# Kernel tuning notes

Measured on AMD Instinct MI355X. Metric: run time of the kernel, lower is better.

## Reference

```python
import jax, jax.numpy as jnp
import numpy as np

D_MODEL = 768
N_HEADS = 4
N_POINTS = 4
PATCH = 16
IMG = 224
HF = IMG // PATCH  # 14
WF = IMG // PATCH  # 14
LQ = HF * WF       # 196 tokens
DH = D_MODEL // N_HEADS  # 192


def setup_inputs() -> dict:
    key = jax.random.key(0)
    ks = jax.random.split(key, 14)
    s = 0.02
    inp = {
        "x": jax.random.normal(ks[0], (4, 16, 3, IMG, IMG), dtype=jnp.float32),
        # patch-embed conv (Conv2d 3->768, k=16, s=16)
        "embed_w": s * jax.random.normal(ks[1], (D_MODEL, 3, PATCH, PATCH), dtype=jnp.float32),
        "embed_b": jnp.zeros((D_MODEL,), dtype=jnp.float32),
        # MSDeformAttn linears (nn.Linear stores W as [out, in]; y = x @ W.T + b)
        "value_w": s * jax.random.normal(ks[2], (D_MODEL, D_MODEL), dtype=jnp.float32),
        "value_b": jnp.zeros((D_MODEL,), dtype=jnp.float32),
        "off_w": s * jax.random.normal(ks[3], (N_HEADS * N_POINTS * 2, D_MODEL), dtype=jnp.float32),
        "off_b": s * jax.random.normal(ks[4], (N_HEADS * N_POINTS * 2,), dtype=jnp.float32),
        "aw_w": s * jax.random.normal(ks[5], (N_HEADS * N_POINTS, D_MODEL), dtype=jnp.float32),
        "aw_b": jnp.zeros((N_HEADS * N_POINTS,), dtype=jnp.float32),
        "outp_w": s * jax.random.normal(ks[6], (D_MODEL, D_MODEL), dtype=jnp.float32),
        "outp_b": jnp.zeros((D_MODEL,), dtype=jnp.float32),
        # final nn.Linear proj
        "proj_w": s * jax.random.normal(ks[7], (D_MODEL, D_MODEL), dtype=jnp.float32),
        "proj_b": jnp.zeros((D_MODEL,), dtype=jnp.float32),
    }
    return inp


def _patch_embed(x, w, b):
    # x: (N,3,H,W); non-overlapping 16x16 patches == Conv2d(3,D,16,16)
    N = x.shape[0]
    xh = x.reshape(N, 3, HF, PATCH, WF, PATCH)
    feat = jnp.einsum('nchpwq,dcpq->nhwd', xh, w) + b  # (N,HF,WF,D)
    return feat.reshape(N, LQ, D_MODEL)


def _ref_points():
    lin = jnp.linspace(0.0, 1.0, HF)
    gy, gx = jnp.meshgrid(lin, lin, indexing='ij')
    return jnp.stack([gx, gy], -1).reshape(LQ, 2)  # (Lq, 2) in [0,1], (x,y)


def _deform_attn_core(value, loc, attn):
    # value: (N, Lq, M, Dh); loc: (N, Lq, M, P, 2) normalized [0,1]; attn: (N, Lq, M, P)
    N = value.shape[0]
    # grid_sample align_corners=False: pixel = (2*loc-1 + 1)*S/2 - 0.5 = loc*S - 0.5
    px = loc[..., 0] * WF - 0.5
    py = loc[..., 1] * HF - 0.5
    x0 = jnp.floor(px).astype(jnp.int32)
    y0 = jnp.floor(py).astype(jnp.int32)
    x1, y1 = x0 + 1, y0 + 1
    wx1 = px - x0.astype(px.dtype)
    wy1 = py - y0.astype(py.dtype)
    wx0, wy0 = 1.0 - wx1, 1.0 - wy1

    valh = value.transpose(0, 2, 1, 3)  # (N, M, HW, Dh)

    def gather(ix, iy):
        valid = (ix >= 0) & (ix < WF) & (iy >= 0) & (iy < HF)  # zeros padding
        idx = jnp.clip(iy, 0, HF - 1) * WF + jnp.clip(ix, 0, WF - 1)
        idxm = idx.transpose(0, 2, 1, 3).reshape(N, N_HEADS, LQ * N_POINTS)
        g = jnp.take_along_axis(valh, idxm[..., None], axis=2)  # (N,M,Lq*P,Dh)
        g = g * valid.transpose(0, 2, 1, 3).reshape(N, N_HEADS, LQ * N_POINTS, 1)
        return g.reshape(N, N_HEADS, LQ, N_POINTS, DH)

    def w4(a, b):  # (N,Lq,M,P) -> (N,M,Lq,P,1)
        return (a * b).transpose(0, 2, 1, 3)[..., None]

    sampled = (w4(wx0, wy0) * gather(x0, y0) + w4(wx1, wy0) * gather(x1, y0)
               + w4(wx0, wy1) * gather(x0, y1) + w4(wx1, wy1) * gather(x1, y1))
    # weighted combine over points
    out = (sampled * attn.transpose(0, 2, 1, 3)[..., None]).sum(3)  # (N,M,Lq,Dh)
    return out.transpose(0, 2, 1, 3).reshape(N, LQ, D_MODEL)


def reference(x, embed_w, embed_b, value_w, value_b, off_w, off_b, aw_w, aw_b,
              outp_w, outp_b, proj_w, proj_b):
    B, T = x.shape[0], x.shape[1]
    N = B * T
    xi = x.reshape(N, 3, IMG, IMG)
    feat = _patch_embed(xi, embed_w, embed_b)  # (N, Lq, D)

    # MSDeformAttn (n_levels=1)
    value = (feat @ value_w.T + value_b).reshape(N, LQ, N_HEADS, DH)
    off = (feat @ off_w.T + off_b).reshape(N, LQ, N_HEADS, N_POINTS, 2)
    aw = (feat @ aw_w.T + aw_b).reshape(N, LQ, N_HEADS, N_POINTS)
    aw = jax.nn.softmax(aw, axis=-1)  # softmax over n_levels*n_points = 4

    ref = _ref_points()  # (Lq, 2)
    norm = jnp.array([WF, HF], dtype=feat.dtype)  # offset_normalizer = (W, H)
    loc = ref[None, :, None, None, :] + off / norm  # (N,Lq,M,P,2)

    out = _deform_attn_core(value, loc, aw)
    out = out @ outp_w.T + outp_b  # output_proj

    pooled = out.mean(axis=1)  # mean over tokens
    final = pooled @ proj_w.T + proj_b
    return final.reshape(B, T, D_MODEL)
```

## Files before the change

kernel.cpp:

```cpp
#include <hip/hip_runtime.h>
#include <hip/hip_bf16.h>


using bf16 = __bf16;
typedef bf16  bf16x4 __attribute__((ext_vector_type(4)));
typedef bf16  bf16x8 __attribute__((ext_vector_type(8)));
typedef float f32x4  __attribute__((ext_vector_type(4)));

#define N_IMG   64
#define LQ      196
#define DM      768
#define NH      4
#define DH      192
#define M_ROWS  (N_IMG * LQ)
#define NCAT    896

#define P_WET    0
#define P_WCAT   288
#define P_BCAT   624
#define P_ZERO   628
#define PREP_GRID 676

#define B_WGEMM   0
#define B_IM2COL  42
#define STAGE_GRID (B_IM2COL + 9408)

#define OFF_A     ((size_t)0)
#define OFF_WC    (OFF_A     + 19267584)
#define OFF_BCAT  (OFF_WC    + 1376256)
#define OFF_VBUF  (OFF_BCAT  + 4096)
#define OFF_OA    (OFF_VBUF  + 19267584)
#define OFF_CORE  (OFF_OA    + 3211264)
#define OFF_POOL  (OFF_CORE  + 196608)
#define OFF_WCATB (OFF_POOL  + 196608)
#define OFF_WET   (OFF_WCATB + 1376256)

__device__ __forceinline__ void gload_lds16(const bf16* g, bf16* l) {
#if __has_builtin(__builtin_amdgcn_global_load_lds)
  __builtin_amdgcn_global_load_lds(
      (const __attribute__((address_space(1))) void*)g,
      (__attribute__((address_space(3))) void*)l, 16, 0, 0);
#else
  *(bf16x8*)l = *(const bf16x8*)g;
#endif
}

__global__ void prep_kernel(const float* __restrict__ embed_w,
                            const float* __restrict__ embed_b,
                            const float* __restrict__ value_w,
                            const float* __restrict__ off_w,
                            const float* __restrict__ aw_w,
                            const float* __restrict__ value_b,
                            const float* __restrict__ off_b,
                            const float* __restrict__ aw_b,
                            bf16* __restrict__ WeT,
                            bf16* __restrict__ Wcatb,
                            float* __restrict__ bcat2,
                            float* __restrict__ core) {
  const int bid = blockIdx.x;
  const int tid = threadIdx.x;

  if (bid < P_WCAT) {
    const int t = bid * 256 + tid;
    const int e = t / 96;
    const int g = t - e * 96;
    bf16x8 o;
#pragma unroll
    for (int j = 0; j < 8; ++j)
      o[j] = (bf16)embed_w[(size_t)(g * 8 + j) * DM + e];
    *(bf16x8*)(WeT + (size_t)e * DM + g * 8) = o;
    return;
  }

  if (bid < P_BCAT) {
    const int t = (bid - P_WCAT) * 256 + tid;
    const int rr = t / 96;
    const int g  = t - rr * 96;
    const float* src = (rr < 768) ? value_w + (size_t)rr * DM
                     : (rr < 800) ? off_w + (size_t)(rr - 768) * DM
                     : (rr < 816) ? aw_w + (size_t)(rr - 800) * DM : nullptr;
    bf16x8 o;
    if (src) {
      const float4 f0 = *(const float4*)(src + g * 8);
      const float4 f1 = *(const float4*)(src + g * 8 + 4);
      o[0] = (bf16)f0.x; o[1] = (bf16)f0.y; o[2] = (bf16)f0.z; o[3] = (bf16)f0.w;
      o[4] = (bf16)f1.x; o[5] = (bf16)f1.y; o[6] = (bf16)f1.z; o[7] = (bf16)f1.w;
    } else {
#pragma unroll
      for (int j = 0; j < 8; ++j) o[j] = (bf16)0.f;
    }
    *(bf16x8*)(Wcatb + (size_t)rr * DM + g * 8) = o;
    return;
  }

  if (bid < P_ZERO) {
    const int o = (bid - P_BCAT) * 256 + tid;
    if (o < NCAT) {
      float bias_o = (o < 768) ? value_b[o]
                   : (o < 800) ? off_b[o - 768]
                   : (o < 816) ? aw_b[o - 800] : 0.f;
      float acc = 0.f;
      if (o < 816) {
        const float* wr = (o < 768) ? value_w + (size_t)o * DM
                        : (o < 800) ? off_w + (size_t)(o - 768) * DM
                        : aw_w + (size_t)(o - 800) * DM;
        const float4* w4p = (const float4*)wr;
        const float4* b4p = (const float4*)embed_b;
#pragma unroll 4
        for (int k = 0; k < DM / 4; ++k) {
          const float4 wv = w4p[k], bv = b4p[k];
          acc += wv.x * bv.x + wv.y * bv.y + wv.z * bv.z + wv.w * bv.w;
        }
      }
      bcat2[o] = acc + bias_o;
    }
    return;
  }

  const int i = (bid - P_ZERO) * 256 + tid;
  f32x4 z = {0.f, 0.f, 0.f, 0.f};
  ((f32x4*)core)[i] = z;
}

__global__ void stage_kernel(const float* __restrict__ x,
                             const bf16* __restrict__ Wcatb,
                             const bf16* __restrict__ WeT,
                             bf16* __restrict__ A,
                             bf16* __restrict__ Wc) {
  const int bid = blockIdx.x;
  const int tid = threadIdx.x;

  if (bid >= B_IM2COL) {
    const int t   = (bid - B_IM2COL) * 256 + tid;
    const int row = t / 192;
    const int j   = t - row * 192;
    const int k   = j * 4;
    const int c   = k >> 8;
    const int r   = k & 255;
    const int p   = r >> 4;
    const int q   = r & 15;
    const int n   = row / 196;
    const int lq  = row - n * 196;
    const int h   = lq / 14;
    const int w   = lq - h * 14;
    const float4 v = *(const float4*)(x +
        ((((size_t)n * 3 + c) * 224) + h * 16 + p) * 224 + w * 16 + q);
    bf16x4 o;
    o[0] = (bf16)v.x; o[1] = (bf16)v.y; o[2] = (bf16)v.z; o[3] = (bf16)v.w;
    *(bf16x4*)(A + (size_t)row * DM + k) = o;
    return;
  }

  const int mT = bid / 6;
  const int nT = bid - mT * 6;
  const int oBase = mT * 128;
  const int eBase = nT * 128;
  const int wave = tid >> 6;
  const int lane = tid & 63;
  const int quad = lane >> 4;
  const int r16  = lane & 15;
  const int wm = wave & 1;
  const int wn = wave >> 1;

  const f32x4 zero = {0.f, 0.f, 0.f, 0.f};
  f32x4 acc[4][4];
#pragma unroll
  for (int mi = 0; mi < 4; ++mi)
#pragma unroll
    for (int ni = 0; ni < 4; ++ni) acc[mi][ni] = zero;

  const bf16* Ab = Wcatb + (size_t)(oBase + wm * 64 + r16) * DM + quad * 8;
  const bf16* Bb = WeT   + (size_t)(eBase + wn * 64 + r16) * DM + quad * 8;

#pragma unroll 2
  for (int kk = 0; kk < DM; kk += 32) {
    bf16x8 af[4], bfr[4];
#pragma unroll
    for (int mi = 0; mi < 4; ++mi)
      af[mi] = *(const bf16x8*)(Ab + (size_t)mi * 16 * DM + kk);
#pragma unroll
    for (int ni = 0; ni < 4; ++ni)
      bfr[ni] = *(const bf16x8*)(Bb + (size_t)ni * 16 * DM + kk);
#pragma unroll
    for (int mi = 0; mi < 4; ++mi)
#pragma unroll
      for (int ni = 0; ni < 4; ++ni)
        acc[mi][ni] = __builtin_amdgcn_mfma_f32_16x16x32_bf16(
            af[mi], bfr[ni], acc[mi][ni], 0, 0, 0);
  }

#pragma unroll
  for (int ni = 0; ni < 4; ++ni) {
    const int col = eBase + wn * 64 + ni * 16 + r16;
#pragma unroll
    for (int mi = 0; mi < 4; ++mi) {
      const int row0 = oBase + wm * 64 + mi * 16 + quad * 4;
#pragma unroll
      for (int rr = 0; rr < 4; ++rr)
        Wc[(size_t)(row0 + rr) * DM + col] = (bf16)acc[mi][ni][rr];
    }
  }
}

__global__ void gemm2_mixed(const bf16* __restrict__ A, const bf16* __restrict__ B,
                            const float* __restrict__ bias,
                            bf16* __restrict__ Vb, float* __restrict__ OA,
                            int M, int N, int K) {
  __shared__ bf16 As[128 * 64];
  __shared__ bf16 Bs[128 * 64];

  const int tid  = threadIdx.x;
  const int wave = tid >> 6;
  const int lane = tid & 63;

  const int p   = blockIdx.y * gridDim.x + blockIdx.x;
  const int nwg = gridDim.x * gridDim.y;
  const int q   = nwg >> 3;
  const int r   = nwg & 7;
  const int xcd = p & 7;
  const int jj  = p >> 3;
  const int L   = (xcd < r ? xcd * (q + 1) : r * (q + 1) + (xcd - r) * q) + jj;
  const int nT  = L % gridDim.x;
  const int mT  = L / gridDim.x;
  const int nBase = nT * 128;
  const int mBase = mT * 128;

  const int wm = wave & 1;
  const int wn = wave >> 1;
  const int quad = lane >> 4;
  const int r16  = lane & 15;

  const f32x4 zero = {0.f, 0.f, 0.f, 0.f};
  f32x4 acc[4][4];
#pragma unroll
  for (int mi = 0; mi < 4; ++mi)
#pragma unroll
    for (int ni = 0; ni < 4; ++ni) acc[mi][ni] = zero;

  const int srow = wave * 32 + (lane >> 3);
  const int scol = (lane & 7) * 8;
  const bf16* Ag = A + (size_t)(mBase + srow) * K + scol;
  const bf16* Bg = B + (size_t)(nBase + srow) * K + scol;
  bf16* Al = As + srow * 64 + scol;
  bf16* Bl = Bs + srow * 64 + scol;

  for (int kt = 0; kt < K; kt += 64) {
#pragma unroll
    for (int i = 0; i < 4; ++i) {
      gload_lds16(Ag + (size_t)(i * 8) * K + kt, Al + i * 8 * 64);
      gload_lds16(Bg + (size_t)(i * 8) * K + kt, Bl + i * 8 * 64);
    }
    __syncthreads();
#pragma unroll
    for (int kk = 0; kk < 64; kk += 32) {
      bf16x8 af[4], bfr[4];
#pragma unroll
      for (int mi = 0; mi < 4; ++mi)
        af[mi] = *(const bf16x8*)&As[(wm * 64 + mi * 16 + r16) * 64 + kk + quad * 8];
#pragma unroll
      for (int ni = 0; ni < 4; ++ni)
        bfr[ni] = *(const bf16x8*)&Bs[(wn * 64 + ni * 16 + r16) * 64 + kk + quad * 8];
#pragma unroll
      for (int mi = 0; mi < 4; ++mi)
#pragma unroll
        for (int ni = 0; ni < 4; ++ni)
          acc[mi][ni] = __builtin_amdgcn_mfma_f32_16x16x32_bf16(
              af[mi], bfr[ni], acc[mi][ni], 0, 0, 0);
    }
    __syncthreads();
  }

#pragma unroll
  for (int ni = 0; ni < 4; ++ni) {
    const int col = nBase + wn * 64 + ni * 16 + r16;
    const float bv = bias[col];
#pragma unroll
    for (int mi = 0; mi < 4; ++mi) {
      const int row0 = mBase + wm * 64 + mi * 16 + quad * 4;
#pragma unroll
      for (int rr = 0; rr < 4; ++rr) {
        float v = acc[mi][ni][rr] + bv;
        int row = row0 + rr;
        if (col < 768) {
          Vb[(size_t)row * 768 + col] = (bf16)v;
        } else if (col < 816) {
          OA[(size_t)row * 64 + (col - 768)] = v;
        }
      }
    }
  }
}

__global__ void deform_kernel(const bf16* __restrict__ Vb,
                              const float* __restrict__ OA,
                              float* __restrict__ core) {
  __shared__ float s_w[64][4];
  __shared__ int   s_t[64][4];

  const int n   = blockIdx.x;
  const int lq0 = blockIdx.y * 4;
  const int z   = blockIdx.z;
  const int tid = threadIdx.x;

  if (tid < 64) {
    const int i = tid >> 4;
    const int m = (tid >> 2) & 3;
    const int p = tid & 3;
    const int lq = lq0 + i;
    const float* row = OA + ((size_t)n * LQ + lq) * 64;

    const float l0 = row[32 + m * 4 + 0];
    const float l1 = row[32 + m * 4 + 1];
    const float l2 = row[32 + m * 4 + 2];
    const float l3 = row[32 + m * 4 + 3];
    const float mx = fmaxf(fmaxf(l0, l1), fmaxf(l2, l3));
    const float e0 = __expf(l0 - mx), e1 = __expf(l1 - mx);
    const float e2 = __expf(l2 - mx), e3 = __expf(l3 - mx);
    const float inv = 1.f / (e0 + e1 + e2 + e3);
    const float ep[4] = {e0, e1, e2, e3};
    const float ew = ep[p] * inv;

    const int h = lq / 14, w = lq - (lq / 14) * 14;
    const float px = (float)w * (14.f / 13.f) - 0.5f + row[(m * 4 + p) * 2 + 0];
    const float py = (float)h * (14.f / 13.f) - 0.5f + row[(m * 4 + p) * 2 + 1];
    const float fx = floorf(px), fy = floorf(py);
    const int x0 = (int)fx, y0 = (int)fy;
    const float wx1 = px - fx, wy1 = py - fy;
    const float wx0 = 1.f - wx1, wy0 = 1.f - wy1;

    const bool vx0 = (x0 >= 0) & (x0 < 14);
    const bool vx1 = (x0 >= -1) & (x0 < 13);
    const bool vy0 = (y0 >= 0) & (y0 < 14);
    const bool vy1 = (y0 >= -1) & (y0 < 13);
    const int cx0 = min(max(x0, 0), 13),      cx1 = min(max(x0 + 1, 0), 13);
    const int cy0 = min(max(y0, 0), 13) * 14, cy1 = min(max(y0 + 1, 0), 13) * 14;

    s_w[tid][0] = (vx0 & vy0) ? ew * wx0 * wy0 : 0.f;
    s_w[tid][1] = (vx1 & vy0) ? ew * wx1 * wy0 : 0.f;
    s_w[tid][2] = (vx0 & vy1) ? ew * wx0 * wy1 : 0.f;
    s_w[tid][3] = (vx1 & vy1) ? ew * wx1 * wy1 : 0.f;
    s_t[tid][0] = cy0 + cx0;
    s_t[tid][1] = cy0 + cx1;
    s_t[tid][2] = cy1 + cx0;
    s_t[tid][3] = cy1 + cx1;
  }
  __syncthreads();

  const int ch = z * 256 + tid;
  const int m  = ch / DH;
  const bf16* vb = Vb + (size_t)n * LQ * 768 + ch;
  float acc = 0.f;
#pragma unroll
  for (int i = 0; i < 4; ++i) {
#pragma unroll
    for (int p = 0; p < 4; ++p) {
      const int e = i * 16 + m * 4 + p;
      const float4 w4 = *(const float4*)s_w[e];
      const int4   t4 = *(const int4*)s_t[e];
      acc += w4.x * (float)vb[(size_t)t4.x * 768];
      acc += w4.y * (float)vb[(size_t)t4.y * 768];
      acc += w4.z * (float)vb[(size_t)t4.z * 768];
      acc += w4.w * (float)vb[(size_t)t4.w * 768];
    }
  }
  atomicAdd(&core[(size_t)n * DM + ch], acc * (1.f / 196.f));
}

__global__ void small_linear_ks(const float* __restrict__ in,
                                const float* __restrict__ W,
                                const float* __restrict__ b,
                                float* __restrict__ out) {
  __shared__ float s_in[4 * DM];
  __shared__ float s_red[3][4][64];
  const int tid = threadIdx.x;
  const int n0 = blockIdx.x * 4;
  const float4* src = (const float4*)(in + (size_t)n0 * DM);
#pragma unroll
  for (int i = 0; i < 3; ++i)
    ((float4*)s_in)[tid + i * 256] = src[tid + i * 256];
  __syncthreads();

  const int dl = tid & 63;
  const int ks = tid >> 6;
  const int d  = blockIdx.y * 64 + dl;
  const int k0 = ks * (DM / 4);

  const float4* w4p = (const float4*)(W + (size_t)d * DM + k0);
  const float4* s0 = (const float4*)(s_in + k0);
  const float4* s1 = (const float4*)(s_in + DM + k0);
  const float4* s2 = (const float4*)(s_in + 2 * DM + k0);
  const float4* s3 = (const float4*)(s_in + 3 * DM + k0);
  float a0 = 0.f, a1 = 0.f, a2 = 0.f, a3 = 0.f;
#pragma unroll 8
  for (int k = 0; k < DM / 16; ++k) {
    const float4 w = w4p[k];
    const float4 v0 = s0[k], v1 = s1[k], v2 = s2[k], v3 = s3[k];
    a0 += w.x * v0.x + w.y * v0.y + w.z * v0.z + w.w * v0.w;
    a1 += w.x * v1.x + w.y * v1.y + w.z * v1.z + w.w * v1.w;
    a2 += w.x * v2.x + w.y * v2.y + w.z * v2.z + w.w * v2.w;
    a3 += w.x * v3.x + w.y * v3.y + w.z * v3.z + w.w * v3.w;
  }

  if (ks > 0) {
    s_red[ks - 1][0][dl] = a0;
    s_red[ks - 1][1][dl] = a1;
    s_red[ks - 1][2][dl] = a2;
    s_red[ks - 1][3][dl] = a3;
  }
  __syncthreads();
  if (ks == 0) {
#pragma unroll
    for (int w = 0; w < 3; ++w) {
      a0 += s_red[w][0][dl];
      a1 += s_red[w][1][dl];
      a2 += s_red[w][2][dl];
      a3 += s_red[w][3][dl];
    }
    const float bv = b[d];
    out[(size_t)(n0 + 0) * DM + d] = a0 + bv;
    out[(size_t)(n0 + 1) * DM + d] = a1 + bv;
    out[(size_t)(n0 + 2) * DM + d] = a2 + bv;
    out[(size_t)(n0 + 3) * DM + d] = a3 + bv;
  }
}

extern "C" void kernel_launch(void* const* d_in, const int* in_sizes, int n_in,
                              void* d_out, int out_size, void* d_ws, size_t ws_size,
                              hipStream_t stream) {
  const float* x       = (const float*)d_in[0];
  const float* embed_w = (const float*)d_in[1];
  const float* embed_b = (const float*)d_in[2];
  const float* value_w = (const float*)d_in[3];
  const float* value_b = (const float*)d_in[4];
  const float* off_w   = (const float*)d_in[5];
  const float* off_b   = (const float*)d_in[6];
  const float* aw_w    = (const float*)d_in[7];
  const float* aw_b    = (const float*)d_in[8];
  const float* outp_w  = (const float*)d_in[9];
  const float* outp_b  = (const float*)d_in[10];
  const float* proj_w  = (const float*)d_in[11];
  const float* proj_b  = (const float*)d_in[12];
  float* out = (float*)d_out;

  char* ws = (char*)d_ws;
  bf16*  A      = (bf16*)(ws + OFF_A);
  bf16*  Wc     = (bf16*)(ws + OFF_WC);
  float* bcat2  = (float*)(ws + OFF_BCAT);
  bf16*  Vbuf   = (bf16*)(ws + OFF_VBUF);
  float* OA     = (float*)(ws + OFF_OA);
  float* core   = (float*)(ws + OFF_CORE);
  float* pooled = (float*)(ws + OFF_POOL);
  bf16*  Wcatb  = (bf16*)(ws + OFF_WCATB);
  bf16*  WeT    = (bf16*)(ws + OFF_WET);

  prep_kernel<<<dim3(PREP_GRID), dim3(256), 0, stream>>>(
      embed_w, embed_b, value_w, off_w, aw_w, value_b, off_b, aw_b,
      WeT, Wcatb, bcat2, core);

  stage_kernel<<<dim3(STAGE_GRID), dim3(256), 0, stream>>>(
      x, Wcatb, WeT, A, Wc);

  gemm2_mixed<<<dim3(NCAT / 128, M_ROWS / 128), dim3(256), 0, stream>>>(
      A, Wc, bcat2, Vbuf, OA, M_ROWS, NCAT, DM);

  deform_kernel<<<dim3(N_IMG, 49, 3), dim3(256), 0, stream>>>(Vbuf, OA, core);

  small_linear_ks<<<dim3(N_IMG / 4, DM / 64), dim3(256), 0, stream>>>(
      core, outp_w, outp_b, pooled);
  small_linear_ks<<<dim3(N_IMG / 4, DM / 64), dim3(256), 0, stream>>>(
      pooled, proj_w, proj_b, out);
}
```

Before: 231.6 us.

## Halve GEMM row tile and vectorize deform sampling over four channels

The fused value/offset GEMM now uses 64x128 tiles instead of 128x128, which doubles the number of workgroups. This aims to balance load across the GPU's compute units, at the cost of less reuse of the B tile per block. The deformable sampling kernel now runs one 192-thread block per (image, 4-query) group, with each thread reading four contiguous bf16 channels per tap, instead of three 256-thread blocks with scalar loads. That cuts redundant softmax and bilinear-weight setup and issues wider loads, in exchange for four atomics per thread and lower thread-level parallelism.

```diff
diff --git a/kernel.cpp b/kernel.cpp
--- a/kernel.cpp
+++ b/kernel.cpp
@@ -206,7 +206,7 @@
                             const float* __restrict__ bias,
                             bf16* __restrict__ Vb, float* __restrict__ OA,
                             int M, int N, int K) {
-  __shared__ bf16 As[128 * 64];
+  __shared__ bf16 As[64 * 64];
   __shared__ bf16 Bs[128 * 64];
 
   const int tid  = threadIdx.x;
@@ -223,7 +223,7 @@
   const int nT  = L % gridDim.x;
   const int mT  = L / gridDim.x;
   const int nBase = nT * 128;
-  const int mBase = mT * 128;
+  const int mBase = mT * 64;
 
   const int wm = wave & 1;
   const int wn = wave >> 1;
@@ -231,37 +231,38 @@
   const int r16  = lane & 15;
 
   const f32x4 zero = {0.f, 0.f, 0.f, 0.f};
-  f32x4 acc[4][4];
-#pragma unroll
-  for (int mi = 0; mi < 4; ++mi)
+  f32x4 acc[2][4];
+#pragma unroll
+  for (int mi = 0; mi < 2; ++mi)
 #pragma unroll
     for (int ni = 0; ni < 4; ++ni) acc[mi][ni] = zero;
 
-  const int srow = wave * 32 + (lane >> 3);
-  const int scol = (lane & 7) * 8;
-  const bf16* Ag = A + (size_t)(mBase + srow) * K + scol;
-  const bf16* Bg = B + (size_t)(nBase + srow) * K + scol;
-  bf16* Al = As + srow * 64 + scol;
-  bf16* Bl = Bs + srow * 64 + scol;
+  const int sr = tid >> 3;
+  const int sc = (tid & 7) * 8;
+  const bf16* Ag = A + (size_t)(mBase + sr) * K + sc;
+  const bf16* Bg = B + (size_t)(nBase + sr) * K + sc;
+  bf16* Al = As + sr * 64 + sc;
+  bf16* Bl = Bs + sr * 64 + sc;
 
   for (int kt = 0; kt < K; kt += 64) {
 #pragma unroll
-    for (int i = 0; i < 4; ++i) {
-      gload_lds16(Ag + (size_t)(i * 8) * K + kt, Al + i * 8 * 64);
-      gload_lds16(Bg + (size_t)(i * 8) * K + kt, Bl + i * 8 * 64);
-    }
+    for (int i = 0; i < 2; ++i)
+      gload_lds16(Ag + (size_t)(i * 32) * K + kt, Al + i * 32 * 64);
+#pragma unroll
+    for (int i = 0; i < 4; ++i)
+      gload_lds16(Bg + (size_t)(i * 32) * K + kt, Bl + i * 32 * 64);
     __syncthreads();
 #pragma unroll
     for (int kk = 0; kk < 64; kk += 32) {
-      bf16x8 af[4], bfr[4];
-#pragma unroll
-      for (int mi = 0; mi < 4; ++mi)
-        af[mi] = *(const bf16x8*)&As[(wm * 64 + mi * 16 + r16) * 64 + kk + quad * 8];
+      bf16x8 af[2], bfr[4];
+#pragma unroll
+      for (int mi = 0; mi < 2; ++mi)
+        af[mi] = *(const bf16x8*)&As[(wm * 32 + mi * 16 + r16) * 64 + kk + quad * 8];
 #pragma unroll
       for (int ni = 0; ni < 4; ++ni)
         bfr[ni] = *(const bf16x8*)&Bs[(wn * 64 + ni * 16 + r16) * 64 + kk + quad * 8];
 #pragma unroll
-      for (int mi = 0; mi < 4; ++mi)
+      for (int mi = 0; mi < 2; ++mi)
 #pragma unroll
         for (int ni = 0; ni < 4; ++ni)
           acc[mi][ni] = __builtin_amdgcn_mfma_f32_16x16x32_bf16(
@@ -275,8 +276,8 @@
     const int col = nBase + wn * 64 + ni * 16 + r16;
     const float bv = bias[col];
 #pragma unroll
-    for (int mi = 0; mi < 4; ++mi) {
-      const int row0 = mBase + wm * 64 + mi * 16 + quad * 4;
+    for (int mi = 0; mi < 2; ++mi) {
+      const int row0 = mBase + wm * 32 + mi * 16 + quad * 4;
 #pragma unroll
       for (int rr = 0; rr < 4; ++rr) {
         float v = acc[mi][ni][rr] + bv;
@@ -299,7 +300,6 @@
 
   const int n   = blockIdx.x;
   const int lq0 = blockIdx.y * 4;
-  const int z   = blockIdx.z;
   const int tid = threadIdx.x;
 
   if (tid < 64) {
@@ -346,10 +346,10 @@
   }
   __syncthreads();
 
-  const int ch = z * 256 + tid;
-  const int m  = ch / DH;
+  const int ch = tid * 4;
+  const int m  = tid / 48;
   const bf16* vb = Vb + (size_t)n * LQ * 768 + ch;
-  float acc = 0.f;
+  float a0 = 0.f, a1 = 0.f, a2 = 0.f, a3 = 0.f;
 #pragma unroll
   for (int i = 0; i < 4; ++i) {
 #pragma unroll
@@ -357,13 +357,25 @@
       const int e = i * 16 + m * 4 + p;
       const float4 w4 = *(const float4*)s_w[e];
       const int4   t4 = *(const int4*)s_t[e];
-      acc += w4.x * (float)vb[(size_t)t4.x * 768];
-      acc += w4.y * (float)vb[(size_t)t4.y * 768];
-      acc += w4.z * (float)vb[(size_t)t4.z * 768];
-      acc += w4.w * (float)vb[(size_t)t4.w * 768];
-    }
-  }
-  atomicAdd(&core[(size_t)n * DM + ch], acc * (1.f / 196.f));
+      const bf16x4 v0 = *(const bf16x4*)(vb + (size_t)t4.x * 768);
+      const bf16x4 v1 = *(const bf16x4*)(vb + (size_t)t4.y * 768);
+      const bf16x4 v2 = *(const bf16x4*)(vb + (size_t)t4.z * 768);
+      const bf16x4 v3 = *(const bf16x4*)(vb + (size_t)t4.w * 768);
+      a0 += w4.x * (float)v0[0] + w4.y * (float)v1[0]
+          + w4.z * (float)v2[0] + w4.w * (float)v3[0];
+      a1 += w4.x * (float)v0[1] + w4.y * (float)v1[1]
+          + w4.z * (float)v2[1] + w4.w * (float)v3[1];
+      a2 += w4.x * (float)v0[2] + w4.y * (float)v1[2]
+          + w4.z * (float)v2[2] + w4.w * (float)v3[2];
+      a3 += w4.x * (float)v0[3] + w4.y * (float)v1[3]
+          + w4.z * (float)v2[3] + w4.w * (float)v3[3];
+    }
+  }
+  float* cp = core + (size_t)n * DM + ch;
+  atomicAdd(cp + 0, a0 * (1.f / 196.f));
+  atomicAdd(cp + 1, a1 * (1.f / 196.f));
+  atomicAdd(cp + 2, a2 * (1.f / 196.f));
+  atomicAdd(cp + 3, a3 * (1.f / 196.f));
 }
 
 __global__ void small_linear_ks(const float* __restrict__ in,
@@ -460,10 +472,10 @@
   stage_kernel<<<dim3(STAGE_GRID), dim3(256), 0, stream>>>(
       x, Wcatb, WeT, A, Wc);
 
-  gemm2_mixed<<<dim3(NCAT / 128, M_ROWS / 128), dim3(256), 0, stream>>>(
+  gemm2_mixed<<<dim3(NCAT / 128, M_ROWS / 64), dim3(256), 0, stream>>>(
       A, Wc, bcat2, Vbuf, OA, M_ROWS, NCAT, DM);
 
-  deform_kernel<<<dim3(N_IMG, 49, 3), dim3(256), 0, stream>>>(Vbuf, OA, core);
+  deform_kernel<<<dim3(N_IMG, 49), dim3(192), 0, stream>>>(Vbuf, OA, core);
 
   small_linear_ks<<<dim3(N_IMG / 4, DM / 64), dim3(256), 0, stream>>>(
       core, outp_w, outp_b, pooled);
```

After: 255.0 us. 1.1x slower.
